# Optimization experiments

Measured on AMD Instinct MI355X. Metric: run time of the kernel, lower is better.

## Reference

```python
import jax, jax.numpy as jnp
import numpy as np

# --- dims (match init_kwargs) ---
B, T, S, K = 4, 128, 64, 2
CS = 1024            # codebook_size
NOTE_V, PHON_V = 128, 64
NE, PE, SE, PGB, PGE = 128, 128, 16, 8, 32
COND, TOK, PREV, D = 256, 256, 256, 512
NH, L_CTX, L_AUD = 8, 4, 6
HIST_WIN, AUD_WIN = 32, 64
DFF = 4 * D

CTX_KEYS = ["ln1_w","ln1_b","in_w","in_b","out_w","out_b","ln2_w","ln2_b","f1_w","f1_b","f2_w","f2_b"]


def _ln(x, w, b):
    m = x.mean(-1, keepdims=True)
    v = ((x - m) ** 2).mean(-1, keepdims=True)
    return (x - m) / jnp.sqrt(v + 1e-5) * w + b


def _mlp2(x, w1, b1, w2, b2, act):
    return act(x @ w1.T + b1) @ w2.T + b2


def _local_mask(n, win):
    i = jnp.arange(n)
    d = i[:, None] - i[None, :]
    return (d < 0) | (d >= win)   # True = masked (causal, local window)


def _mha(x, mask, in_w, in_b, out_w, out_b, nh):
    b, s, d = x.shape
    dh = d // nh
    q, k, v = jnp.split(x @ in_w.T + in_b, 3, axis=-1)
    sp = lambda t: t.reshape(b, s, nh, dh).transpose(0, 2, 1, 3)
    q, k, v = sp(q), sp(k), sp(v)
    sc = jnp.einsum('bhqd,bhkd->bhqk', q, k) * (1.0 / np.sqrt(dh))
    sc = jnp.where(mask, -1e9, sc)
    a = jax.nn.softmax(sc, axis=-1)
    o = jnp.einsum('bhqk,bhkd->bhqd', a, v).transpose(0, 2, 1, 3).reshape(b, s, d)
    return o @ out_w.T + out_b


def _block(x, mask, pr, nh):
    # pr: dict with ln1_w..f2_b for one layer (pre-norm attn + FFN, GELU)
    h = _ln(x, pr["ln1_w"], pr["ln1_b"])
    x = x + _mha(h, mask, pr["in_w"], pr["in_b"], pr["out_w"], pr["out_b"], nh)
    h2 = _ln(x, pr["ln2_w"], pr["ln2_b"])
    return x + _mlp2(h2, pr["f1_w"], pr["f1_b"], pr["f2_w"], pr["f2_b"],
                     lambda z: jax.nn.gelu(z, approximate=False))


def _forward(p, codes, note_id, phoneme_id, slur, phone_progress):
    silu = jax.nn.silu
    # ---- condition encoder ----
    cond_in = jnp.concatenate([
        p["note_emb_w"][note_id], p["phoneme_emb_w"][phoneme_id],
        p["slur_emb_w"][jnp.clip(slur, 0, 1)], p["pp_emb_w"][phone_progress]], -1)
    cond = _mlp2(cond_in, p["cond_w1"], p["cond_b1"], p["cond_w2"], p["cond_b2"], silu)
    # ---- shifted prev-step representation ----
    first = codes[..., 0]                       # [B,T,S]
    pooled = p["token_emb_w"][first].mean(2)    # [B,T,TOK]
    prev = _mlp2(pooled, p["prev_w1"], p["prev_b1"], p["prev_w2"], p["prev_b2"], silu)
    bos = jnp.broadcast_to(p["bos_step"], (B, 1, PREV))
    prev = jnp.concatenate([bos, prev[:, :-1]], 1)
    # ---- context transformer over steps (local causal window) ----
    h = _mlp2(jnp.concatenate([cond, prev], -1), p["step_w1"], p["step_b1"], p["step_w2"], p["step_b2"], silu)
    m_ctx = _local_mask(T, HIST_WIN)
    for l in range(L_CTX):
        pr = {k: p["ctx_" + k][l] for k in CTX_KEYS}
        h = _block(h, m_ctx, pr, NH)
    # ---- audio decoder over frames within each step ----
    tok = p["token_emb_w"][first] @ p["audio_in_w"].T + p["audio_in_b"]   # [B,T,S,D]
    bos_a = jnp.broadcast_to(p["audio_bos"], (B, T, 1, D))
    a = jnp.concatenate([bos_a, tok[:, :, :-1]], 2) + p["frame_pos"][None, None] + h[:, :, None]
    a = a.reshape(B * T, S, D)
    m_a = _local_mask(S, min(AUD_WIN, S))
    for l in range(L_AUD):
        pr = {k: p["aud_" + k][l] for k in CTX_KEYS}
        a = _block(a, m_a, pr, NH)
    ah = a.reshape(B, T, S, D)
    # ---- heads ----
    first_logits = (ah @ p["first_w"].T + p["first_b"])[..., None, :]     # [B,T,S,1,CS]
    rh = _mlp2(jnp.concatenate([ah, tok], -1), p["resc_w1"], p["resc_b1"], p["resc_w2"], p["resc_b2"], silu)
    res = jnp.einsum('btsd,kcd->btskc', rh, p["res_w"]) + p["res_b"]       # [B,T,S,K-1,CS]
    return jnp.concatenate([first_logits, res], axis=3)                    # [B,T,S,K,CS]


def setup_inputs() -> dict:
    key = jax.random.key(0)
    ks = iter(jax.random.split(key, 128))
    w = lambda *sh: jax.random.normal(next(ks), sh, jnp.float32) * 0.02
    z = lambda *sh: jnp.zeros(sh, jnp.float32)
    o = lambda *sh: jnp.ones(sh, jnp.float32)
    inp = {
        "codes": jax.random.randint(next(ks), (B, T, S, K), 0, CS, jnp.int32),
        "note_id": jax.random.randint(next(ks), (B, T), 0, NOTE_V, jnp.int32),
        "phoneme_id": jax.random.randint(next(ks), (B, T), 0, PHON_V, jnp.int32),
        "slur": jax.random.randint(next(ks), (B, T), 0, 2, jnp.int32),
        "phone_progress": jax.random.randint(next(ks), (B, T), 0, PGB, jnp.int32),
        "note_emb_w": w(NOTE_V, NE), "phoneme_emb_w": w(PHON_V, PE),
        "slur_emb_w": w(2, SE), "pp_emb_w": w(PGB, PGE),
        "cond_w1": w(COND, NE + PE + SE + PGE), "cond_b1": z(COND),
        "cond_w2": w(COND, COND), "cond_b2": z(COND),
        "token_emb_w": w(CS, TOK),
        "prev_w1": w(PREV, TOK), "prev_b1": z(PREV),
        "prev_w2": w(PREV, PREV), "prev_b2": z(PREV),
        "bos_step": z(PREV),
        "step_w1": w(D, COND + PREV), "step_b1": z(D),
        "step_w2": w(D, D), "step_b2": z(D),
        "audio_in_w": w(D, TOK), "audio_in_b": z(D),
        "audio_bos": z(D), "frame_pos": w(S, D),
        "first_w": w(CS, D), "first_b": z(CS),
        "resc_w1": w(D, 2 * D), "resc_b1": z(D),
        "resc_w2": w(D, D), "resc_b2": z(D),
        "res_w": w(K - 1, CS, D), "res_b": z(K - 1, CS),
    }
    for pre, L in (("ctx_", L_CTX), ("aud_", L_AUD)):
        inp[pre + "ln1_w"] = o(L, D); inp[pre + "ln1_b"] = z(L, D)
        inp[pre + "in_w"] = w(L, 3 * D, D); inp[pre + "in_b"] = z(L, 3 * D)
        inp[pre + "out_w"] = w(L, D, D); inp[pre + "out_b"] = z(L, D)
        inp[pre + "ln2_w"] = o(L, D); inp[pre + "ln2_b"] = z(L, D)
        inp[pre + "f1_w"] = w(L, DFF, D); inp[pre + "f1_b"] = z(L, DFF)
        inp[pre + "f2_w"] = w(L, D, DFF); inp[pre + "f2_b"] = z(L, D)
    return inp


FLOAT_KEYS = ["note_emb_w","phoneme_emb_w","slur_emb_w","pp_emb_w","cond_w1","cond_b1","cond_w2","cond_b2","token_emb_w","prev_w1","prev_b1","prev_w2","prev_b2","bos_step","step_w1","step_b1","step_w2","step_b2","audio_in_w","audio_in_b","audio_bos","frame_pos","first_w","first_b","resc_w1","resc_b1","resc_w2","resc_b2","res_w","res_b"] + [p + k for p in ("ctx_","aud_") for k in CTX_KEYS]


def reference(codes, note_id, phoneme_id, slur, phone_progress,
              note_emb_w, phoneme_emb_w, slur_emb_w, pp_emb_w,
              cond_w1, cond_b1, cond_w2, cond_b2, token_emb_w,
              prev_w1, prev_b1, prev_w2, prev_b2, bos_step,
              step_w1, step_b1, step_w2, step_b2,
              audio_in_w, audio_in_b, audio_bos, frame_pos,
              first_w, first_b, resc_w1, resc_b1, resc_w2, resc_b2, res_w, res_b,
              ctx_ln1_w, ctx_ln1_b, ctx_in_w, ctx_in_b, ctx_out_w, ctx_out_b,
              ctx_ln2_w, ctx_ln2_b, ctx_f1_w, ctx_f1_b, ctx_f2_w, ctx_f2_b,
              aud_ln1_w, aud_ln1_b, aud_in_w, aud_in_b, aud_out_w, aud_out_b,
              aud_ln2_w, aud_ln2_b, aud_f1_w, aud_f1_b, aud_f2_w, aud_f2_b):
    loc = locals()
    p = {k: loc[k] for k in FLOAT_KEYS}
    return _forward(p, codes, note_id, phoneme_id, slur, phone_progress)
```

## Files before the change

### kernel.cpp

```cpp
#include <hip/hip_runtime.h>
#include <cstdint>
#include <cstddef>

typedef unsigned short u16;
typedef short bf16x8 __attribute__((ext_vector_type(8)));
typedef float f32x4 __attribute__((ext_vector_type(4)));

__device__ __forceinline__ float bf2f(u16 u) { return __uint_as_float(((unsigned)u) << 16); }
__device__ __forceinline__ u16 f2bf(float f) {
  unsigned i = __float_as_uint(f);
  i += 0x7fffu + ((i >> 16) & 1u);
  return (u16)(i >> 16);
}
__device__ __forceinline__ unsigned packbf2(float lo, float hi) {
  return (unsigned)f2bf(lo) | ((unsigned)f2bf(hi) << 16);
}
__device__ __forceinline__ float lo16(unsigned u) { return __uint_as_float(u << 16); }
__device__ __forceinline__ float hi16(unsigned u) { return __uint_as_float(u & 0xffff0000u); }

__device__ __forceinline__ void async_ld16(u16* lds, const u16* g) {
  __builtin_amdgcn_global_load_lds((const __attribute__((address_space(1))) void*)g,
                                   (__attribute__((address_space(3))) void*)lds, 16, 0, 0);
}

__device__ __forceinline__ void fbar() {
  __builtin_amdgcn_sched_barrier(0);
  __builtin_amdgcn_s_barrier();
  __builtin_amdgcn_sched_barrier(0);
}

__global__ void k_cast8(const float4* __restrict__ x, uint4* __restrict__ y, int n8) {
  int i = blockIdx.x * 256 + threadIdx.x;
  if (i >= n8) return;
  float4 a = x[(size_t)i * 2], b = x[(size_t)i * 2 + 1];
  uint4 o;
  o.x = packbf2(a.x, a.y); o.y = packbf2(a.z, a.w);
  o.z = packbf2(b.x, b.y); o.w = packbf2(b.z, b.w);
  y[i] = o;
}

template<int ACT, int OUTM>
__global__ __launch_bounds__(256)
void gemm_mfma(const u16* __restrict__ A, const u16* __restrict__ W,
               const float* __restrict__ bias, void* __restrict__ Cp,
               int M, int N, int K, int ldc) {
  __shared__ __align__(16) u16 SM[24576];
  const int tid = threadIdx.x;
  const int wave = tid >> 6, lane = tid & 63;

  const int gx = gridDim.x;
  const int nwg = gx * (int)gridDim.y;
  const int flat = (int)blockIdx.y * gx + (int)blockIdx.x;
  const int xcd = flat & 7, lo = flat >> 3;
  const int q = nwg >> 3, r = nwg & 7;
  const int swz = (xcd < r ? xcd * (q + 1) : r * (q + 1) + (xcd - r) * q) + lo;
  const int bm = (swz / gx) * 128, bn = (swz % gx) * 128;

  const int wm = (wave & 1) * 64, wn = (wave >> 1) * 64;
  const int srow = tid >> 2, selem = (tid & 3) * 8;
  const u16* Ap0 = A + (size_t)(bm + srow) * K + selem;
  const u16* Ap1 = A + (size_t)(bm + srow + 64) * K + selem;
  const u16* Wp0 = W + (size_t)(bn + srow) * K + selem;
  const u16* Wp1 = W + (size_t)(bn + srow + 64) * K + selem;
  const int fr = lane & 15, fq = (lane >> 4) * 8;

  f32x4 acc[4][4];
#pragma unroll
  for (int i = 0; i < 4; ++i)
#pragma unroll
    for (int j = 0; j < 4; ++j) acc[i][j] = (f32x4){0.f, 0.f, 0.f, 0.f};

  const int nt = K >> 5;

  auto stage = [&](int buf, int k0) {
    u16* AsD = SM + buf * 4096 + tid * 8;
    u16* BsD = SM + 12288 + buf * 4096 + tid * 8;
    async_ld16(AsD, Ap0 + k0);
    async_ld16(AsD + 2048, Ap1 + k0);
    async_ld16(BsD, Wp0 + k0);
    async_ld16(BsD + 2048, Wp1 + k0);
  };

  stage(0, 0);
  if (nt > 1) stage(1, 32);

  int bi = 0;
  for (int t = 0; t < nt; ++t) {
    if (t + 1 < nt) asm volatile("s_waitcnt vmcnt(4)" ::: "memory");
    else            asm volatile("s_waitcnt vmcnt(0)" ::: "memory");
    __builtin_amdgcn_s_barrier();
    if (t + 2 < nt) {
      int nb = bi + 2; if (nb >= 3) nb -= 3;
      stage(nb, (t + 2) << 5);
    }
    const u16* Asb = SM + bi * 4096;
    const u16* Bsb = SM + 12288 + bi * 4096;
    bf16x8 af[4], bfv[4];
#pragma unroll
    for (int i = 0; i < 4; ++i)
      af[i] = *(const bf16x8*)&Asb[(wm + i * 16 + fr) * 32 + fq];
#pragma unroll
    for (int j = 0; j < 4; ++j)
      bfv[j] = *(const bf16x8*)&Bsb[(wn + j * 16 + fr) * 32 + fq];
#pragma unroll
    for (int i = 0; i < 4; ++i)
#pragma unroll
      for (int j = 0; j < 4; ++j)
        acc[i][j] = __builtin_amdgcn_mfma_f32_16x16x32_bf16(af[i], bfv[j], acc[i][j], 0, 0, 0);
    if (++bi == 3) bi = 0;
  }

  __syncthreads();
  const int lrow = (lane >> 4) * 4;
  const int colb = wn + fr;

  if (OUTM == 0) {
    u16* Ep = SM;
#pragma unroll
    for (int j = 0; j < 4; ++j) {
      float bv = bias[bn + colb + j * 16];
#pragma unroll
      for (int i = 0; i < 4; ++i)
#pragma unroll
        for (int rr = 0; rr < 4; ++rr) {
          float v = acc[i][j][rr] + bv;
          if (ACT == 1) v = v / (1.f + __expf(-v));
          else if (ACT == 2) v = 0.5f * v * (1.f + erff(v * 0.70710678118f));
          Ep[(wm + i * 16 + lrow + rr) * 128 + colb + j * 16] = f2bf(v);
        }
    }
    __syncthreads();
#pragma unroll
    for (int it = 0; it < 8; ++it) {
      int idx = it * 256 + tid;
      int row = idx >> 4, c = idx & 15;
      *(uint4*)((u16*)Cp + (size_t)(bm + row) * ldc + bn + c * 8) =
          ((const uint4*)Ep)[idx];
    }
  } else {
    float* Ep = (float*)SM;
    float* Cf = (float*)Cp;
#pragma unroll
    for (int ch = 0; ch < 2; ++ch) {
      if ((wave & 1) == ch) {
#pragma unroll
        for (int j = 0; j < 4; ++j) {
          float bv = bias[bn + colb + j * 16];
#pragma unroll
          for (int i = 0; i < 4; ++i)
#pragma unroll
            for (int rr = 0; rr < 4; ++rr) {
              float v = acc[i][j][rr] + bv;
              if (ACT == 1) v = v / (1.f + __expf(-v));
              else if (ACT == 2) v = 0.5f * v * (1.f + erff(v * 0.70710678118f));
              Ep[(i * 16 + lrow + rr) * 128 + colb + j * 16] = v;
            }
        }
      }
      __syncthreads();
#pragma unroll
      for (int it = 0; it < 8; ++it) {
        int idx = it * 256 + tid;
        int row = idx >> 5, c4 = idx & 31;
        size_t g = (size_t)(bm + ch * 64 + row) * ldc + bn + c4 * 4;
        float4 sv = ((const float4*)Ep)[idx];
        if (OUTM == 1) {
          float4 od = *(const float4*)(Cf + g);
          sv.x += od.x; sv.y += od.y; sv.z += od.z; sv.w += od.w;
        }
        *(float4*)(Cf + g) = sv;
      }
      __syncthreads();
    }
  }
}

template<int ACT, int OUTM>
__global__ __launch_bounds__(512, 2)
void gemm_mfma256(const u16* __restrict__ A, const u16* __restrict__ W,
                  const float* __restrict__ bias, void* __restrict__ Cp,
                  int M, int N, int K, int ldc) {
  __shared__ __align__(16) u16 SM[65536];
  const int tid = threadIdx.x;
  const int wave = tid >> 6, lane = tid & 63;
  const int wave_m = wave >> 2, wave_n = wave & 3;
  const int WM = wave_m * 128, WN = wave_n * 64;

  const int gx = gridDim.x;
  const int nwg = gx * (int)gridDim.y;
  const int flat = (int)blockIdx.y * gx + (int)blockIdx.x;
  const int xcd = flat & 7, lo = flat >> 3;
  const int q = nwg >> 3, r = nwg & 7;
  const int swz = (xcd < r ? xcd * (q + 1) : r * (q + 1) + (xcd - r) * q) + lo;
  const int bm = (swz / gx) * 256, bn = (swz % gx) * 256;

  const int srow = tid >> 3;
  const int slc = (tid & 7) ^ (srow & 7);
  const u16* Asrc = A + (size_t)(bm + srow) * K + slc * 8;
  const u16* Wsrc = W + (size_t)(bn + srow) * K + slc * 8;

  auto stage = [&](int buf, int k0) {
    u16* Ad = SM + buf * 32768 + tid * 8;
    u16* Bd = SM + buf * 32768 + 16384 + tid * 8;
#pragma unroll
    for (int qq = 0; qq < 4; ++qq)
      async_ld16(Ad + qq * 4096, Asrc + (size_t)qq * 64 * K + k0);
#pragma unroll
    for (int qq = 0; qq < 4; ++qq)
      async_ld16(Bd + qq * 4096, Wsrc + (size_t)qq * 64 * K + k0);
  };

  const int fr = lane & 15;
  const int pc0 = (((lane >> 4) ^ (fr & 7))) * 8;
  const int arow0 = (WM + fr) * 64;
  const int brow0 = (WN + fr) * 64;

  f32x4 acc[8][4];
#pragma unroll
  for (int i = 0; i < 8; ++i)
#pragma unroll
    for (int j = 0; j < 4; ++j) acc[i][j] = (f32x4){0.f, 0.f, 0.f, 0.f};

  const int nt = K >> 6;

  stage(0, 0);
  if (nt > 1) stage(1, 64);

  bf16x8 aA[4][2], bB[4][2];

#pragma unroll 1
  for (int t = 0; t < nt; ++t) {
    const u16* Ab = SM + (t & 1) * 32768;
    const u16* Bb = Ab + 16384;
    if (t + 1 < nt) asm volatile("s_waitcnt vmcnt(8)" ::: "memory");
    else            asm volatile("s_waitcnt vmcnt(0)" ::: "memory");
    fbar();
#pragma unroll
    for (int mi = 0; mi < 4; ++mi)
#pragma unroll
      for (int ks = 0; ks < 2; ++ks)
        aA[mi][ks] = *(const bf16x8*)&Ab[arow0 + mi * 1024 + (pc0 ^ (ks * 32))];
#pragma unroll
    for (int nj = 0; nj < 2; ++nj)
#pragma unroll
      for (int ks = 0; ks < 2; ++ks)
        bB[nj][ks] = *(const bf16x8*)&Bb[brow0 + nj * 1024 + (pc0 ^ (ks * 32))];
    __builtin_amdgcn_s_setprio(1);
#pragma unroll
    for (int mi = 0; mi < 4; ++mi)
#pragma unroll
      for (int nj = 0; nj < 2; ++nj)
#pragma unroll
        for (int ks = 0; ks < 2; ++ks)
          acc[mi][nj] = __builtin_amdgcn_mfma_f32_16x16x32_bf16(aA[mi][ks], bB[nj][ks], acc[mi][nj], 0, 0, 0);
    __builtin_amdgcn_s_setprio(0);
    fbar();
#pragma unroll
    for (int nj = 2; nj < 4; ++nj)
#pragma unroll
      for (int ks = 0; ks < 2; ++ks)
        bB[nj][ks] = *(const bf16x8*)&Bb[brow0 + nj * 1024 + (pc0 ^ (ks * 32))];
    __builtin_amdgcn_s_setprio(1);
#pragma unroll
    for (int mi = 0; mi < 4; ++mi)
#pragma unroll
      for (int nj = 2; nj < 4; ++nj)
#pragma unroll
        for (int ks = 0; ks < 2; ++ks)
          acc[mi][nj] = __builtin_amdgcn_mfma_f32_16x16x32_bf16(aA[mi][ks], bB[nj][ks], acc[mi][nj], 0, 0, 0);
    __builtin_amdgcn_s_setprio(0);
    fbar();
#pragma unroll
    for (int mi = 0; mi < 4; ++mi)
#pragma unroll
      for (int ks = 0; ks < 2; ++ks)
        aA[mi][ks] = *(const bf16x8*)&Ab[arow0 + (mi + 4) * 1024 + (pc0 ^ (ks * 32))];
    __builtin_amdgcn_s_setprio(1);
#pragma unroll
    for (int mi = 0; mi < 4; ++mi)
#pragma unroll
      for (int nj = 2; nj < 4; ++nj)
#pragma unroll
        for (int ks = 0; ks < 2; ++ks)
          acc[mi + 4][nj] = __builtin_amdgcn_mfma_f32_16x16x32_bf16(aA[mi][ks], bB[nj][ks], acc[mi + 4][nj], 0, 0, 0);
    __builtin_amdgcn_s_setprio(0);
    fbar();
    if (t + 2 < nt) stage(t & 1, (t + 2) << 6);
    __builtin_amdgcn_s_setprio(1);
#pragma unroll
    for (int mi = 0; mi < 4; ++mi)
#pragma unroll
      for (int nj = 0; nj < 2; ++nj)
#pragma unroll
        for (int ks = 0; ks < 2; ++ks)
          acc[mi + 4][nj] = __builtin_amdgcn_mfma_f32_16x16x32_bf16(aA[mi][ks], bB[nj][ks], acc[mi + 4][nj], 0, 0, 0);
    __builtin_amdgcn_s_setprio(0);
  }

  fbar();
  const int lrow = (lane >> 4) * 4;
  const int colb = WN + fr;

  if (OUTM == 0) {
    u16* Ep = SM;
#pragma unroll
    for (int nj = 0; nj < 4; ++nj) {
      float bv = bias[bn + colb + nj * 16];
#pragma unroll
      for (int mi = 0; mi < 8; ++mi)
#pragma unroll
        for (int rr = 0; rr < 4; ++rr) {
          float v = acc[mi][nj][rr] + bv;
          if (ACT == 1) v = v / (1.f + __expf(-v));
          else if (ACT == 2) v = 0.5f * v * (1.f + erff(v * 0.70710678118f));
          Ep[(WM + mi * 16 + lrow + rr) * 256 + colb + nj * 16] = f2bf(v);
        }
    }
    __syncthreads();
#pragma unroll
    for (int it = 0; it < 16; ++it) {
      int idx = it * 512 + tid;
      int row = idx >> 5, c = idx & 31;
      *(uint4*)((u16*)Cp + (size_t)(bm + row) * ldc + bn + c * 8) =
          ((const uint4*)Ep)[idx];
    }
  } else {
    float* Ep = (float*)SM;
    float* Cf = (float*)Cp;
#pragma unroll
    for (int ch = 0; ch < 2; ++ch) {
      if (wave_m == ch) {
#pragma unroll
        for (int nj = 0; nj < 4; ++nj) {
          float bv = bias[bn + colb + nj * 16];
#pragma unroll
          for (int mi = 0; mi < 8; ++mi)
#pragma unroll
            for (int rr = 0; rr < 4; ++rr) {
              float v = acc[mi][nj][rr] + bv;
              if (ACT == 1) v = v / (1.f + __expf(-v));
              else if (ACT == 2) v = 0.5f * v * (1.f + erff(v * 0.70710678118f));
              Ep[(mi * 16 + lrow + rr) * 256 + colb + nj * 16] = v;
            }
        }
      }
      __syncthreads();
#pragma unroll
      for (int it = 0; it < 16; ++it) {
        int idx = it * 512 + tid;
        int row = idx >> 6, c4 = idx & 63;
        size_t g = (size_t)(bm + ch * 128 + row) * ldc + bn + c4 * 4;
        float4 sv = ((const float4*)Ep)[idx];
        if (OUTM == 1) {
          float4 od = *(const float4*)(Cf + g);
          sv.x += od.x; sv.y += od.y; sv.z += od.z; sv.w += od.w;
        }
        *(float4*)(Cf + g) = sv;
      }
      __syncthreads();
    }
  }
}

__global__ __launch_bounds__(256)
void k_layernorm(const float* __restrict__ X, const float* __restrict__ w,
                 const float* __restrict__ b, u16* __restrict__ Y) {
  int row = blockIdx.x, tid = threadIdx.x;
  const float* x = X + (size_t)row * 512;
  float v0 = x[tid], v1 = x[tid + 256];
  __shared__ float red[4];
  float s = v0 + v1;
  for (int o = 32; o; o >>= 1) s += __shfl_down(s, o, 64);
  if ((tid & 63) == 0) red[tid >> 6] = s;
  __syncthreads();
  if (tid == 0) red[0] = (red[0] + red[1] + red[2] + red[3]) * (1.f / 512.f);
  __syncthreads();
  float mean = red[0];
  __syncthreads();
  float d0 = v0 - mean, d1 = v1 - mean;
  float q = d0 * d0 + d1 * d1;
  for (int o = 32; o; o >>= 1) q += __shfl_down(q, o, 64);
  if ((tid & 63) == 0) red[tid >> 6] = q;
  __syncthreads();
  if (tid == 0) red[0] = (red[0] + red[1] + red[2] + red[3]) * (1.f / 512.f);
  __syncthreads();
  float rstd = rsqrtf(red[0] + 1e-5f);
  size_t o0 = (size_t)row * 512 + tid;
  Y[o0] = f2bf(d0 * rstd * w[tid] + b[tid]);
  Y[o0 + 256] = f2bf(d1 * rstd * w[tid + 256] + b[tid + 256]);
}

__global__ void k_cond_gather(const int* __restrict__ note_id, const int* __restrict__ phon_id,
                              const int* __restrict__ slur, const int* __restrict__ pp,
                              const float* __restrict__ note_emb, const float* __restrict__ phon_emb,
                              const float* __restrict__ slur_emb, const float* __restrict__ pp_emb,
                              u16* __restrict__ out) {
  int bt = blockIdx.x, t = threadIdx.x;
  u16 v = 0;
  if (t < 128) v = f2bf(note_emb[note_id[bt] * 128 + t]);
  else if (t < 256) v = f2bf(phon_emb[phon_id[bt] * 128 + (t - 128)]);
  else if (t < 272) {
    int sv = slur[bt]; sv = sv < 0 ? 0 : (sv > 1 ? 1 : sv);
    v = f2bf(slur_emb[sv * 16 + (t - 256)]);
  } else if (t < 304) v = f2bf(pp_emb[pp[bt] * 32 + (t - 272)]);
  out[bt * 320 + t] = v;
}

__global__ void k_pad_w(const float* __restrict__ w, u16* __restrict__ out) {
  int n = blockIdx.x, t = threadIdx.x;
  out[n * 320 + t] = (t < 304) ? f2bf(w[n * 304 + t]) : (u16)0;
}

__global__ void k_femb(const int* __restrict__ codes, const uint4* __restrict__ emb,
                       uint4* __restrict__ out) {
  int i = blockIdx.x * 256 + threadIdx.x;
  int m = i >> 5, c = i & 31;
  out[i] = emb[(size_t)codes[m * 2] * 32 + c];
}

__global__ void k_pool(const u16* __restrict__ femb, u16* __restrict__ pooled) {
  int bt = blockIdx.x, c = threadIdx.x;
  float s = 0.f;
  for (int j = 0; j < 64; ++j) s += bf2f(femb[((size_t)bt * 64 + j) * 256 + c]);
  pooled[bt * 256 + c] = f2bf(s * (1.f / 64.f));
}

__global__ void k_stepin(const u16* __restrict__ cond, const u16* __restrict__ prevo,
                         const float* __restrict__ bosf, u16* __restrict__ out) {
  int bt = blockIdx.x, t = threadIdx.x;
  u16 v;
  if (t < 256) v = cond[bt * 256 + t];
  else {
    int tt = bt & 127;
    v = (tt == 0) ? f2bf(bosf[t - 256]) : prevo[(bt - 1) * 256 + (t - 256)];
  }
  out[bt * 512 + t] = v;
}

__global__ __launch_bounds__(64)
void k_ctx_attn(const u16* __restrict__ qkv, u16* __restrict__ out) {
  int t = blockIdx.x, h = blockIdx.y, b = blockIdx.z;
  int lane = threadIdx.x;
  int bt = b * 128 + t;
  float qd = bf2f(qkv[(size_t)bt * 1536 + h * 64 + lane]) * 0.125f;
  int klo = t - 31; if (klo < 0) klo = 0;
  int n = t - klo + 1;
  __shared__ float sc[32];
  for (int i = 0; i < n; ++i) {
    float p = qd * bf2f(qkv[((size_t)(b * 128 + klo + i)) * 1536 + 512 + h * 64 + lane]);
    for (int o = 32; o; o >>= 1) p += __shfl_xor(p, o, 64);
    if (lane == 0) sc[i] = p;
  }
  __syncthreads();
  float mx = -1e30f;
  for (int i = 0; i < n; ++i) mx = fmaxf(mx, sc[i]);
  float den = 0.f, acc = 0.f;
  for (int i = 0; i < n; ++i) {
    float p = __expf(sc[i] - mx);
    den += p;
    acc += p * bf2f(qkv[((size_t)(b * 128 + klo + i)) * 1536 + 1024 + h * 64 + lane]);
  }
  out[(size_t)bt * 512 + h * 64 + lane] = f2bf(acc / den);
}

__global__ __launch_bounds__(128)
void k_aud_attn_mfma(const u16* __restrict__ qkv, u16* __restrict__ out) {
  constexpr int LP = 66;
  __shared__ u16 Pl[2][64 * LP];
  __shared__ u16 Vt[2][64 * LP];
  const int wave = threadIdx.x >> 6, lane = threadIdx.x & 63;
  const int id = blockIdx.x * 2 + wave;
  const int seq = id >> 3, h = id & 7;
  const u16* Qb = qkv + (size_t)seq * 64 * 1536 + h * 64;
  const u16* Kb = Qb + 512;
  const u16* Vb = Qb + 1024;
  u16* Plw = Pl[wave];
  u16* Vtw = Vt[wave];
  const int fr = lane & 15, fq = (lane >> 4) * 8;

#pragma unroll
  for (int t = 0; t < 8; ++t) {
    int vr = (lane >> 3) + 8 * t, vc = (lane & 7) * 8;
    uint4 vv = *(const uint4*)(Vb + (size_t)vr * 1536 + vc);
    Vtw[(vc + 0) * LP + vr] = (u16)(vv.x & 0xffff);
    Vtw[(vc + 1) * LP + vr] = (u16)(vv.x >> 16);
    Vtw[(vc + 2) * LP + vr] = (u16)(vv.y & 0xffff);
    Vtw[(vc + 3) * LP + vr] = (u16)(vv.y >> 16);
    Vtw[(vc + 4) * LP + vr] = (u16)(vv.z & 0xffff);
    Vtw[(vc + 5) * LP + vr] = (u16)(vv.z >> 16);
    Vtw[(vc + 6) * LP + vr] = (u16)(vv.w & 0xffff);
    Vtw[(vc + 7) * LP + vr] = (u16)(vv.w >> 16);
  }

  bf16x8 aq[4][2], bk[4][2];
#pragma unroll
  for (int i = 0; i < 4; ++i)
#pragma unroll
    for (int c = 0; c < 2; ++c) {
      aq[i][c] = *(const bf16x8*)(Qb + (size_t)(i * 16 + fr) * 1536 + fq + 32 * c);
      bk[i][c] = *(const bf16x8*)(Kb + (size_t)(i * 16 + fr) * 1536 + fq + 32 * c);
    }
  f32x4 s[4][4];
#pragma unroll
  for (int i = 0; i < 4; ++i)
#pragma unroll
    for (int j = 0; j < 4; ++j) s[i][j] = (f32x4){0.f, 0.f, 0.f, 0.f};
#pragma unroll
  for (int c = 0; c < 2; ++c)
#pragma unroll
    for (int i = 0; i < 4; ++i)
#pragma unroll
      for (int j = 0; j < 4; ++j)
        s[i][j] = __builtin_amdgcn_mfma_f32_16x16x32_bf16(aq[i][c], bk[j][c], s[i][j], 0, 0, 0);

  const int qr = (lane >> 4) * 4;
#pragma unroll
  for (int i = 0; i < 4; ++i) {
#pragma unroll
    for (int r = 0; r < 4; ++r) {
      int row = 16 * i + qr + r;
      float mx = -1e30f;
      float vj[4];
#pragma unroll
      for (int j = 0; j < 4; ++j) {
        float v = s[i][j][r] * 0.125f;
        if (16 * j + fr > row) v = -1e30f;
        vj[j] = v;
        mx = fmaxf(mx, v);
      }
      for (int o = 8; o; o >>= 1) mx = fmaxf(mx, __shfl_xor(mx, o, 64));
      float den = 0.f;
#pragma unroll
      for (int j = 0; j < 4; ++j) { vj[j] = __expf(vj[j] - mx); den += vj[j]; }
      for (int o = 8; o; o >>= 1) den += __shfl_xor(den, o, 64);
      float inv = 1.f / den;
#pragma unroll
      for (int j = 0; j < 4; ++j)
        Plw[row * LP + 16 * j + fr] = f2bf(vj[j] * inv);
    }
  }
  __syncthreads();

  f32x4 o4[4][4];
#pragma unroll
  for (int i = 0; i < 4; ++i)
#pragma unroll
    for (int j = 0; j < 4; ++j) o4[i][j] = (f32x4){0.f, 0.f, 0.f, 0.f};
#pragma unroll
  for (int c = 0; c < 2; ++c) {
    bf16x8 ap[4], bv[4];
#pragma unroll
    for (int i = 0; i < 4; ++i)
      ap[i] = *(const bf16x8*)&Plw[(16 * i + fr) * LP + fq + 32 * c];
#pragma unroll
    for (int j = 0; j < 4; ++j)
      bv[j] = *(const bf16x8*)&Vtw[(16 * j + fr) * LP + fq + 32 * c];
#pragma unroll
    for (int i = 0; i < 4; ++i)
#pragma unroll
      for (int j = 0; j < 4; ++j)
        o4[i][j] = __builtin_amdgcn_mfma_f32_16x16x32_bf16(ap[i], bv[j], o4[i][j], 0, 0, 0);
  }
#pragma unroll
  for (int i = 0; i < 4; ++i)
#pragma unroll
    for (int r = 0; r < 4; ++r) {
      int row = 16 * i + qr + r;
      u16* ob = out + ((size_t)seq * 64 + row) * 512 + h * 64;
#pragma unroll
      for (int j = 0; j < 4; ++j) ob[16 * j + fr] = f2bf(o4[i][j][r]);
    }
}

__global__ void k_abuild(const uint4* __restrict__ tok, const float4* __restrict__ bosf,
                         const float4* __restrict__ fpos, const float4* __restrict__ hstep,
                         float4* __restrict__ a) {
  size_t i = (size_t)blockIdx.x * 256 + threadIdx.x;
  int d8 = (int)(i & 63);
  size_t row = i >> 6;
  int s = (int)(row & 63);
  size_t bt = row >> 6;
  float t0, t1, t2, t3, t4, t5, t6, t7;
  if (s == 0) {
    float4 b0 = bosf[d8 * 2], b1 = bosf[d8 * 2 + 1];
    t0 = b0.x; t1 = b0.y; t2 = b0.z; t3 = b0.w;
    t4 = b1.x; t5 = b1.y; t6 = b1.z; t7 = b1.w;
  } else {
    uint4 tv = tok[(row - 1) * 64 + d8];
    t0 = lo16(tv.x); t1 = hi16(tv.x); t2 = lo16(tv.y); t3 = hi16(tv.y);
    t4 = lo16(tv.z); t5 = hi16(tv.z); t6 = lo16(tv.w); t7 = hi16(tv.w);
  }
  float4 f0 = fpos[(size_t)s * 128 + d8 * 2], f1 = fpos[(size_t)s * 128 + d8 * 2 + 1];
  float4 h0 = hstep[bt * 128 + d8 * 2], h1 = hstep[bt * 128 + d8 * 2 + 1];
  float4 o0, o1;
  o0.x = t0 + f0.x + h0.x; o0.y = t1 + f0.y + h0.y;
  o0.z = t2 + f0.z + h0.z; o0.w = t3 + f0.w + h0.w;
  o1.x = t4 + f1.x + h1.x; o1.y = t5 + f1.y + h1.y;
  o1.z = t6 + f1.z + h1.z; o1.w = t7 + f1.w + h1.w;
  a[i * 2] = o0; a[i * 2 + 1] = o1;
}

__global__ void k_cat(const uint4* __restrict__ ah, const uint4* __restrict__ tok,
                      uint4* __restrict__ out) {
  size_t i = (size_t)blockIdx.x * 256 + threadIdx.x;
  size_t m = i >> 7;
  int c = (int)(i & 127);
  out[i] = (c < 64) ? ah[m * 64 + c] : tok[m * 64 + (c - 64)];
}

template<int ACT, int OUTM>
static inline void gemm(const u16* A, const u16* W, const float* bias, void* C,
                        int M, int N, int K, int ldc, hipStream_t s) {
  gemm_mfma<ACT, OUTM><<<dim3(N / 128, M / 128), 256, 0, s>>>(A, W, bias, C, M, N, K, ldc);
}

template<int ACT, int OUTM>
static inline void gemmBig(const u16* A, const u16* W, const float* bias, void* C,
                           int M, int N, int K, int ldc, hipStream_t s) {
  gemm_mfma256<ACT, OUTM><<<dim3(N / 256, M / 256), 512, 0, s>>>(A, W, bias, C, M, N, K, ldc);
}

static inline void cast_bf16(const float* x, u16* y, size_t n, hipStream_t s) {
  int n8 = (int)(n / 8);
  k_cast8<<<(n8 + 255) / 256, 256, 0, s>>>((const float4*)x, (uint4*)y, n8);
}

extern "C" void kernel_launch(void* const* d_in, const int* in_sizes, int n_in,
                              void* d_out, int out_size, void* d_ws, size_t ws_size,
                              hipStream_t stream) {
  const int* codes    = (const int*)d_in[0];
  const int* note_id  = (const int*)d_in[1];
  const int* phon_id  = (const int*)d_in[2];
  const int* slur     = (const int*)d_in[3];
  const int* pprog    = (const int*)d_in[4];
  const float* note_emb = (const float*)d_in[5];
  const float* phon_emb = (const float*)d_in[6];
  const float* slur_emb = (const float*)d_in[7];
  const float* pp_emb   = (const float*)d_in[8];
  const float* cond_w1  = (const float*)d_in[9];
  const float* cond_b1  = (const float*)d_in[10];
  const float* cond_w2  = (const float*)d_in[11];
  const float* cond_b2  = (const float*)d_in[12];
  const float* tok_emb  = (const float*)d_in[13];
  const float* prev_w1  = (const float*)d_in[14];
  const float* prev_b1  = (const float*)d_in[15];
  const float* prev_w2  = (const float*)d_in[16];
  const float* prev_b2  = (const float*)d_in[17];
  const float* bos_step = (const float*)d_in[18];
  const float* step_w1  = (const float*)d_in[19];
  const float* step_b1  = (const float*)d_in[20];
  const float* step_w2  = (const float*)d_in[21];
  const float* step_b2  = (const float*)d_in[22];
  const float* audio_in_w = (const float*)d_in[23];
  const float* audio_in_b = (const float*)d_in[24];
  const float* audio_bos  = (const float*)d_in[25];
  const float* frame_pos  = (const float*)d_in[26];
  const float* first_w  = (const float*)d_in[27];
  const float* first_b  = (const float*)d_in[28];
  const float* resc_w1  = (const float*)d_in[29];
  const float* resc_b1  = (const float*)d_in[30];
  const float* resc_w2  = (const float*)d_in[31];
  const float* resc_b2  = (const float*)d_in[32];
  const float* res_w    = (const float*)d_in[33];
  const float* res_b    = (const float*)d_in[34];
  const float* ctx_w[12]; for (int i = 0; i < 12; ++i) ctx_w[i] = (const float*)d_in[35 + i];
  const float* aud_w[12]; for (int i = 0; i < 12; ++i) aud_w[i] = (const float*)d_in[47 + i];

  char* p = (char*)d_ws;
  auto alloc = [&](size_t b) { char* r = p; p += (b + 255) & ~(size_t)255; return r; };
  float* A_res = (float*)alloc(32768ull * 512 * 4);
  u16* T_tok  = (u16*)alloc(32768ull * 512 * 2);
  u16* LNb    = (u16*)alloc(32768ull * 512 * 2);
  u16* AOb    = (u16*)alloc(32768ull * 512 * 2);
  u16* QF     = (u16*)alloc(32768ull * 2048 * 2);
  u16* f_emb  = (u16*)alloc(32768ull * 256 * 2);
  u16* temb   = (u16*)alloc(1024ull * 256 * 2);
  u16* cond_in = (u16*)alloc(512ull * 320 * 2);
  u16* cw1p   = (u16*)alloc(256ull * 320 * 2);
  u16* cw2    = (u16*)alloc(256ull * 256 * 2);
  u16* pw1    = (u16*)alloc(256ull * 256 * 2);
  u16* pw2    = (u16*)alloc(256ull * 256 * 2);
  u16* sw1    = (u16*)alloc(512ull * 512 * 2);
  u16* sw2    = (u16*)alloc(512ull * 512 * 2);
  u16* ainw   = (u16*)alloc(512ull * 256 * 2);
  u16* fw     = (u16*)alloc(1024ull * 512 * 2);
  u16* rw1    = (u16*)alloc(512ull * 1024 * 2);
  u16* rw2    = (u16*)alloc(512ull * 512 * 2);
  u16* resw   = (u16*)alloc(1024ull * 512 * 2);
  u16* cxin   = (u16*)alloc(4ull * 1536 * 512 * 2);
  u16* cxout  = (u16*)alloc(4ull * 512 * 512 * 2);
  u16* cxf1   = (u16*)alloc(4ull * 2048 * 512 * 2);
  u16* cxf2   = (u16*)alloc(4ull * 512 * 2048 * 2);
  u16* adin   = (u16*)alloc(6ull * 1536 * 512 * 2);
  u16* adout  = (u16*)alloc(6ull * 512 * 512 * 2);
  u16* adf1   = (u16*)alloc(6ull * 2048 * 512 * 2);
  u16* adf2   = (u16*)alloc(6ull * 512 * 2048 * 2);
  u16* cond_h = (u16*)alloc(512ull * 256 * 2);
  u16* condv  = (u16*)alloc(512ull * 256 * 2);
  u16* pooled = (u16*)alloc(512ull * 256 * 2);
  u16* prevh  = (u16*)alloc(512ull * 256 * 2);
  u16* prevo  = (u16*)alloc(512ull * 256 * 2);
  u16* stepin = (u16*)alloc(512ull * 512 * 2);
  u16* hmid   = (u16*)alloc(512ull * 512 * 2);
  float* hstep = (float*)alloc(512ull * 512 * 4);

  k_pad_w<<<256, 320, 0, stream>>>(cond_w1, cw1p);
  cast_bf16(cond_w2, cw2, 256ull * 256, stream);
  cast_bf16(prev_w1, pw1, 256ull * 256, stream);
  cast_bf16(prev_w2, pw2, 256ull * 256, stream);
  cast_bf16(step_w1, sw1, 512ull * 512, stream);
  cast_bf16(step_w2, sw2, 512ull * 512, stream);
  cast_bf16(tok_emb, temb, 1024ull * 256, stream);
  cast_bf16(audio_in_w, ainw, 512ull * 256, stream);
  cast_bf16(first_w, fw, 1024ull * 512, stream);
  cast_bf16(resc_w1, rw1, 512ull * 1024, stream);
  cast_bf16(resc_w2, rw2, 512ull * 512, stream);
  cast_bf16(res_w, resw, 1024ull * 512, stream);
  cast_bf16(ctx_w[2], cxin, 4ull * 1536 * 512, stream);
  cast_bf16(ctx_w[4], cxout, 4ull * 512 * 512, stream);
  cast_bf16(ctx_w[8], cxf1, 4ull * 2048 * 512, stream);
  cast_bf16(ctx_w[10], cxf2, 4ull * 512 * 2048, stream);
  cast_bf16(aud_w[2], adin, 6ull * 1536 * 512, stream);
  cast_bf16(aud_w[4], adout, 6ull * 512 * 512, stream);
  cast_bf16(aud_w[8], adf1, 6ull * 2048 * 512, stream);
  cast_bf16(aud_w[10], adf2, 6ull * 512 * 2048, stream);

  k_cond_gather<<<512, 320, 0, stream>>>(note_id, phon_id, slur, pprog,
                                         note_emb, phon_emb, slur_emb, pp_emb, cond_in);
  k_femb<<<4096, 256, 0, stream>>>(codes, (const uint4*)temb, (uint4*)f_emb);
  k_pool<<<512, 256, 0, stream>>>(f_emb, pooled);
  gemm<1, 0>(cond_in, cw1p, cond_b1, cond_h, 512, 256, 320, 256, stream);
  gemm<0, 0>(cond_h, cw2, cond_b2, condv, 512, 256, 256, 256, stream);
  gemm<1, 0>(pooled, pw1, prev_b1, prevh, 512, 256, 256, 256, stream);
  gemm<0, 0>(prevh, pw2, prev_b2, prevo, 512, 256, 256, 256, stream);
  k_stepin<<<512, 512, 0, stream>>>(condv, prevo, bos_step, stepin);
  gemm<1, 0>(stepin, sw1, step_b1, hmid, 512, 512, 512, 512, stream);
  gemm<0, 2>(hmid, sw2, step_b2, hstep, 512, 512, 512, 512, stream);

  for (int l = 0; l < 4; ++l) {
    k_layernorm<<<512, 256, 0, stream>>>(hstep, ctx_w[0] + l * 512, ctx_w[1] + l * 512, LNb);
    gemm<0, 0>(LNb, cxin + (size_t)l * 1536 * 512, ctx_w[3] + l * 1536, QF, 512, 1536, 512, 1536, stream);
    k_ctx_attn<<<dim3(128, 8, 4), 64, 0, stream>>>(QF, AOb);
    gemm<0, 1>(AOb, cxout + (size_t)l * 512 * 512, ctx_w[5] + l * 512, hstep, 512, 512, 512, 512, stream);
    k_layernorm<<<512, 256, 0, stream>>>(hstep, ctx_w[6] + l * 512, ctx_w[7] + l * 512, LNb);
    gemm<2, 0>(LNb, cxf1 + (size_t)l * 2048 * 512, ctx_w[9] + l * 2048, QF, 512, 2048, 512, 2048, stream);
    gemm<0, 1>(QF, cxf2 + (size_t)l * 512 * 2048, ctx_w[11] + l * 512, hstep, 512, 512, 2048, 512, stream);
  }

  gemmBig<0, 0>(f_emb, ainw, audio_in_b, T_tok, 32768, 512, 256, 512, stream);
  k_abuild<<<8192, 256, 0, stream>>>((const uint4*)T_tok, (const float4*)audio_bos,
                                     (const float4*)frame_pos, (const float4*)hstep, (float4*)A_res);
  for (int l = 0; l < 6; ++l) {
    k_layernorm<<<32768, 256, 0, stream>>>(A_res, aud_w[0] + l * 512, aud_w[1] + l * 512, LNb);
    gemmBig<0, 0>(LNb, adin + (size_t)l * 1536 * 512, aud_w[3] + l * 1536, QF, 32768, 1536, 512, 1536, stream);
    k_aud_attn_mfma<<<2048, 128, 0, stream>>>(QF, AOb);
    gemmBig<0, 1>(AOb, adout + (size_t)l * 512 * 512, aud_w[5] + l * 512, A_res, 32768, 512, 512, 512, stream);
    k_layernorm<<<32768, 256, 0, stream>>>(A_res, aud_w[6] + l * 512, aud_w[7] + l * 512, LNb);
    gemmBig<2, 0>(LNb, adf1 + (size_t)l * 2048 * 512, aud_w[9] + l * 2048, QF, 32768, 2048, 512, 2048, stream);
    gemmBig<0, 1>(QF, adf2 + (size_t)l * 512 * 2048, aud_w[11] + l * 512, A_res, 32768, 512, 2048, 512, stream);
  }

  {
    int n8 = 32768 * 512 / 8;
    k_cast8<<<(n8 + 255) / 256, 256, 0, stream>>>((const float4*)A_res, (uint4*)LNb, n8);
  }
  gemmBig<0, 2>(LNb, fw, first_b, (float*)d_out, 32768, 1024, 512, 2048, stream);
  k_cat<<<16384, 256, 0, stream>>>((const uint4*)LNb, (const uint4*)T_tok, (uint4*)QF);
  gemmBig<1, 0>(QF, rw1, resc_b1, AOb, 32768, 512, 1024, 512, stream);
  gemmBig<0, 0>(AOb, rw2, resc_b2, T_tok, 32768, 512, 512, 512, stream);
  gemmBig<0, 2>(T_tok, resw, res_b, (float*)d_out + 1024, 32768, 1024, 512, 2048, stream);
}
```

Before: 3.601 ms.

## Retile small GEMMs to 64x64 and fuse the concat into the residual GEMM load

The M=512 condition, step and context GEMMs move to a new 64x64-tile kernel. It writes results straight from registers, so these small problems launch more workgroups. The residual-head GEMM gains a split-A mode that reads columns 0-511 from one buffer and 512-1023 from another, which removes the separate k_cat kernel and its intermediate buffer. A __syncthreads is also dropped in the audio attention kernel between writing the P tile and the PV stage. That is only safe if each wave reads only its own rows, so it risks a race.

```diff
diff --git a/kernel.cpp b/kernel.cpp
--- a/kernel.cpp
+++ b/kernel.cpp
@@ -41,44 +41,28 @@
 
 template<int ACT, int OUTM>
 __global__ __launch_bounds__(256)
-void gemm_mfma(const u16* __restrict__ A, const u16* __restrict__ W,
-               const float* __restrict__ bias, void* __restrict__ Cp,
-               int M, int N, int K, int ldc) {
-  __shared__ __align__(16) u16 SM[24576];
+void gemm_mfma64(const u16* __restrict__ A, const u16* __restrict__ W,
+                 const float* __restrict__ bias, void* __restrict__ Cp,
+                 int M, int N, int K, int ldc) {
+  __shared__ __align__(16) u16 SM[12288];
   const int tid = threadIdx.x;
   const int wave = tid >> 6, lane = tid & 63;
-
-  const int gx = gridDim.x;
-  const int nwg = gx * (int)gridDim.y;
-  const int flat = (int)blockIdx.y * gx + (int)blockIdx.x;
-  const int xcd = flat & 7, lo = flat >> 3;
-  const int q = nwg >> 3, r = nwg & 7;
-  const int swz = (xcd < r ? xcd * (q + 1) : r * (q + 1) + (xcd - r) * q) + lo;
-  const int bm = (swz / gx) * 128, bn = (swz % gx) * 128;
-
-  const int wm = (wave & 1) * 64, wn = (wave >> 1) * 64;
+  const int bm = blockIdx.y * 64, bn = blockIdx.x * 64;
   const int srow = tid >> 2, selem = (tid & 3) * 8;
-  const u16* Ap0 = A + (size_t)(bm + srow) * K + selem;
-  const u16* Ap1 = A + (size_t)(bm + srow + 64) * K + selem;
-  const u16* Wp0 = W + (size_t)(bn + srow) * K + selem;
-  const u16* Wp1 = W + (size_t)(bn + srow + 64) * K + selem;
+  const u16* Ap = A + (size_t)(bm + srow) * K + selem;
+  const u16* Wp = W + (size_t)(bn + srow) * K + selem;
   const int fr = lane & 15, fq = (lane >> 4) * 8;
-
-  f32x4 acc[4][4];
-#pragma unroll
-  for (int i = 0; i < 4; ++i)
-#pragma unroll
-    for (int j = 0; j < 4; ++j) acc[i][j] = (f32x4){0.f, 0.f, 0.f, 0.f};
+  const int wn = wave * 16;
+
+  f32x4 acc[4];
+#pragma unroll
+  for (int i = 0; i < 4; ++i) acc[i] = (f32x4){0.f, 0.f, 0.f, 0.f};
 
   const int nt = K >> 5;
 
   auto stage = [&](int buf, int k0) {
-    u16* AsD = SM + buf * 4096 + tid * 8;
-    u16* BsD = SM + 12288 + buf * 4096 + tid * 8;
-    async_ld16(AsD, Ap0 + k0);
-    async_ld16(AsD + 2048, Ap1 + k0);
-    async_ld16(BsD, Wp0 + k0);
-    async_ld16(BsD + 2048, Wp1 + k0);
+    async_ld16(SM + buf * 2048 + tid * 8, Ap + k0);
+    async_ld16(SM + 6144 + buf * 2048 + tid * 8, Wp + k0);
   };
 
   stage(0, 0);
@@ -86,98 +70,47 @@
 
   int bi = 0;
   for (int t = 0; t < nt; ++t) {
-    if (t + 1 < nt) asm volatile("s_waitcnt vmcnt(4)" ::: "memory");
+    if (t + 1 < nt) asm volatile("s_waitcnt vmcnt(2)" ::: "memory");
     else            asm volatile("s_waitcnt vmcnt(0)" ::: "memory");
     __builtin_amdgcn_s_barrier();
     if (t + 2 < nt) {
       int nb = bi + 2; if (nb >= 3) nb -= 3;
       stage(nb, (t + 2) << 5);
     }
-    const u16* Asb = SM + bi * 4096;
-    const u16* Bsb = SM + 12288 + bi * 4096;
-    bf16x8 af[4], bfv[4];
+    const u16* Asb = SM + bi * 2048;
+    const u16* Bsb = SM + 6144 + bi * 2048;
+    bf16x8 af[4];
 #pragma unroll
     for (int i = 0; i < 4; ++i)
-      af[i] = *(const bf16x8*)&Asb[(wm + i * 16 + fr) * 32 + fq];
-#pragma unroll
-    for (int j = 0; j < 4; ++j)
-      bfv[j] = *(const bf16x8*)&Bsb[(wn + j * 16 + fr) * 32 + fq];
+      af[i] = *(const bf16x8*)&Asb[(i * 16 + fr) * 32 + fq];
+    bf16x8 bf1 = *(const bf16x8*)&Bsb[(wn + fr) * 32 + fq];
 #pragma unroll
     for (int i = 0; i < 4; ++i)
-#pragma unroll
-      for (int j = 0; j < 4; ++j)
-        acc[i][j] = __builtin_amdgcn_mfma_f32_16x16x32_bf16(af[i], bfv[j], acc[i][j], 0, 0, 0);
+      acc[i] = __builtin_amdgcn_mfma_f32_16x16x32_bf16(af[i], bf1, acc[i], 0, 0, 0);
     if (++bi == 3) bi = 0;
   }
 
-  __syncthreads();
-  const int lrow = (lane >> 4) * 4;
-  const int colb = wn + fr;
-
-  if (OUTM == 0) {
-    u16* Ep = SM;
-#pragma unroll
-    for (int j = 0; j < 4; ++j) {
-      float bv = bias[bn + colb + j * 16];
-#pragma unroll
-      for (int i = 0; i < 4; ++i)
-#pragma unroll
-        for (int rr = 0; rr < 4; ++rr) {
-          float v = acc[i][j][rr] + bv;
-          if (ACT == 1) v = v / (1.f + __expf(-v));
-          else if (ACT == 2) v = 0.5f * v * (1.f + erff(v * 0.70710678118f));
-          Ep[(wm + i * 16 + lrow + rr) * 128 + colb + j * 16] = f2bf(v);
-        }
-    }
-    __syncthreads();
-#pragma unroll
-    for (int it = 0; it < 8; ++it) {
-      int idx = it * 256 + tid;
-      int row = idx >> 4, c = idx & 15;
-      *(uint4*)((u16*)Cp + (size_t)(bm + row) * ldc + bn + c * 8) =
-          ((const uint4*)Ep)[idx];
-    }
-  } else {
-    float* Ep = (float*)SM;
-    float* Cf = (float*)Cp;
-#pragma unroll
-    for (int ch = 0; ch < 2; ++ch) {
-      if ((wave & 1) == ch) {
-#pragma unroll
-        for (int j = 0; j < 4; ++j) {
-          float bv = bias[bn + colb + j * 16];
-#pragma unroll
-          for (int i = 0; i < 4; ++i)
-#pragma unroll
-            for (int rr = 0; rr < 4; ++rr) {
-              float v = acc[i][j][rr] + bv;
-              if (ACT == 1) v = v / (1.f + __expf(-v));
-              else if (ACT == 2) v = 0.5f * v * (1.f + erff(v * 0.70710678118f));
-              Ep[(i * 16 + lrow + rr) * 128 + colb + j * 16] = v;
-            }
-        }
-      }
-      __syncthreads();
-#pragma unroll
-      for (int it = 0; it < 8; ++it) {
-        int idx = it * 256 + tid;
-        int row = idx >> 5, c4 = idx & 31;
-        size_t g = (size_t)(bm + ch * 64 + row) * ldc + bn + c4 * 4;
-        float4 sv = ((const float4*)Ep)[idx];
-        if (OUTM == 1) {
-          float4 od = *(const float4*)(Cf + g);
-          sv.x += od.x; sv.y += od.y; sv.z += od.z; sv.w += od.w;
-        }
-        *(float4*)(Cf + g) = sv;
-      }
-      __syncthreads();
-    }
-  }
-}
-
-template<int ACT, int OUTM>
+  const int mr = bm + (lane >> 4) * 4;
+  const int nc = bn + wn + fr;
+  float bv = bias[nc];
+#pragma unroll
+  for (int i = 0; i < 4; ++i)
+#pragma unroll
+    for (int rr = 0; rr < 4; ++rr) {
+      float v = acc[i][rr] + bv;
+      if (ACT == 1) v = v / (1.f + __expf(-v));
+      else if (ACT == 2) v = 0.5f * v * (1.f + erff(v * 0.70710678118f));
+      size_t off = (size_t)(mr + i * 16 + rr) * ldc + nc;
+      if (OUTM == 0) ((u16*)Cp)[off] = f2bf(v);
+      else if (OUTM == 1) ((float*)Cp)[off] += v;
+      else ((float*)Cp)[off] = v;
+    }
+}
+
+template<int ACT, int OUTM, int SPLITA>
 __global__ __launch_bounds__(512, 2)
-void gemm_mfma256(const u16* __restrict__ A, const u16* __restrict__ W,
+void gemm_mfma256(const u16* __restrict__ A, const u16* __restrict__ A2,
+                  const u16* __restrict__ W,
                   const float* __restrict__ bias, void* __restrict__ Cp,
                   int M, int N, int K, int ldc) {
   __shared__ __align__(16) u16 SM[65536];
@@ -195,16 +128,30 @@
   const int bm = (swz / gx) * 256, bn = (swz % gx) * 256;
 
   const int srow = tid >> 3;
-  const int slc = (tid & 7) ^ (srow & 7);
-  const u16* Asrc = A + (size_t)(bm + srow) * K + slc * 8;
-  const u16* Wsrc = W + (size_t)(bn + srow) * K + slc * 8;
+  const int slc8 = ((tid & 7) ^ (srow & 7)) * 8;
+  const u16* Asrc = nullptr; const u16* A2src = nullptr;
+  if (SPLITA) {
+    Asrc  = A  + (size_t)(bm + srow) * 512;
+    A2src = A2 + (size_t)(bm + srow) * 512 - 512;
+  } else {
+    Asrc = A + (size_t)(bm + srow) * K + slc8;
+  }
+  const u16* Wsrc = W + (size_t)(bn + srow) * K + slc8;
 
   auto stage = [&](int buf, int k0) {
     u16* Ad = SM + buf * 32768 + tid * 8;
-    u16* Bd = SM + buf * 32768 + 16384 + tid * 8;
-#pragma unroll
-    for (int qq = 0; qq < 4; ++qq)
-      async_ld16(Ad + qq * 4096, Asrc + (size_t)qq * 64 * K + k0);
+    u16* Bd = Ad + 16384;
+    if (SPLITA) {
+      int col = k0 + slc8;
+      const u16* s = (col < 512 ? Asrc : A2src) + col;
+#pragma unroll
+      for (int qq = 0; qq < 4; ++qq)
+        async_ld16(Ad + qq * 4096, s + (size_t)qq * 64 * 512);
+    } else {
+#pragma unroll
+      for (int qq = 0; qq < 4; ++qq)
+        async_ld16(Ad + qq * 4096, Asrc + (size_t)qq * 64 * K + k0);
+    }
 #pragma unroll
     for (int qq = 0; qq < 4; ++qq)
       async_ld16(Bd + qq * 4096, Wsrc + (size_t)qq * 64 * K + k0);
@@ -539,7 +486,6 @@
         Plw[row * LP + 16 * j + fr] = f2bf(vj[j] * inv);
     }
   }
-  __syncthreads();
 
   f32x4 o4[4][4];
 #pragma unroll
@@ -600,24 +546,22 @@
   a[i * 2] = o0; a[i * 2 + 1] = o1;
 }
 
-__global__ void k_cat(const uint4* __restrict__ ah, const uint4* __restrict__ tok,
-                      uint4* __restrict__ out) {
-  size_t i = (size_t)blockIdx.x * 256 + threadIdx.x;
-  size_t m = i >> 7;
-  int c = (int)(i & 127);
-  out[i] = (c < 64) ? ah[m * 64 + c] : tok[m * 64 + (c - 64)];
-}
-
 template<int ACT, int OUTM>
-static inline void gemm(const u16* A, const u16* W, const float* bias, void* C,
-                        int M, int N, int K, int ldc, hipStream_t s) {
-  gemm_mfma<ACT, OUTM><<<dim3(N / 128, M / 128), 256, 0, s>>>(A, W, bias, C, M, N, K, ldc);
+static inline void gemmS(const u16* A, const u16* W, const float* bias, void* C,
+                         int M, int N, int K, int ldc, hipStream_t s) {
+  gemm_mfma64<ACT, OUTM><<<dim3(N / 64, M / 64), 256, 0, s>>>(A, W, bias, C, M, N, K, ldc);
 }
 
 template<int ACT, int OUTM>
 static inline void gemmBig(const u16* A, const u16* W, const float* bias, void* C,
                            int M, int N, int K, int ldc, hipStream_t s) {
-  gemm_mfma256<ACT, OUTM><<<dim3(N / 256, M / 256), 512, 0, s>>>(A, W, bias, C, M, N, K, ldc);
+  gemm_mfma256<ACT, OUTM, 0><<<dim3(N / 256, M / 256), 512, 0, s>>>(A, nullptr, W, bias, C, M, N, K, ldc);
+}
+
+template<int ACT, int OUTM>
+static inline void gemmBigSplit(const u16* A, const u16* A2, const u16* W, const float* bias,
+                                void* C, int M, int N, int K, int ldc, hipStream_t s) {
+  gemm_mfma256<ACT, OUTM, 1><<<dim3(N / 256, M / 256), 512, 0, s>>>(A, A2, W, bias, C, M, N, K, ldc);
 }
 
 static inline void cast_bf16(const float* x, u16* y, size_t n, hipStream_t s) {
@@ -729,22 +673,22 @@
                                          note_emb, phon_emb, slur_emb, pp_emb, cond_in);
   k_femb<<<4096, 256, 0, stream>>>(codes, (const uint4*)temb, (uint4*)f_emb);
   k_pool<<<512, 256, 0, stream>>>(f_emb, pooled);
-  gemm<1, 0>(cond_in, cw1p, cond_b1, cond_h, 512, 256, 320, 256, stream);
-  gemm<0, 0>(cond_h, cw2, cond_b2, condv, 512, 256, 256, 256, stream);
-  gemm<1, 0>(pooled, pw1, prev_b1, prevh, 512, 256, 256, 256, stream);
-  gemm<0, 0>(prevh, pw2, prev_b2, prevo, 512, 256, 256, 256, stream);
+  gemmS<1, 0>(cond_in, cw1p, cond_b1, cond_h, 512, 256, 320, 256, stream);
+  gemmS<0, 0>(cond_h, cw2, cond_b2, condv, 512, 256, 256, 256, stream);
+  gemmS<1, 0>(pooled, pw1, prev_b1, prevh, 512, 256, 256, 256, stream);
+  gemmS<0, 0>(prevh, pw2, prev_b2, prevo, 512, 256, 256, 256, stream);
   k_stepin<<<512, 512, 0, stream>>>(condv, prevo, bos_step, stepin);
-  gemm<1, 0>(stepin, sw1, step_b1, hmid, 512, 512, 512, 512, stream);
-  gemm<0, 2>(hmid, sw2, step_b2, hstep, 512, 512, 512, 512, stream);
+  gemmS<1, 0>(stepin, sw1, step_b1, hmid, 512, 512, 512, 512, stream);
+  gemmS<0, 2>(hmid, sw2, step_b2, hstep, 512, 512, 512, 512, stream);
 
   for (int l = 0; l < 4; ++l) {
     k_layernorm<<<512, 256, 0, stream>>>(hstep, ctx_w[0] + l * 512, ctx_w[1] + l * 512, LNb);
-    gemm<0, 0>(LNb, cxin + (size_t)l * 1536 * 512, ctx_w[3] + l * 1536, QF, 512, 1536, 512, 1536, stream);
+    gemmS<0, 0>(LNb, cxin + (size_t)l * 1536 * 512, ctx_w[3] + l * 1536, QF, 512, 1536, 512, 1536, stream);
     k_ctx_attn<<<dim3(128, 8, 4), 64, 0, stream>>>(QF, AOb);
-    gemm<0, 1>(AOb, cxout + (size_t)l * 512 * 512, ctx_w[5] + l * 512, hstep, 512, 512, 512, 512, stream);
+    gemmS<0, 1>(AOb, cxout + (size_t)l * 512 * 512, ctx_w[5] + l * 512, hstep, 512, 512, 512, 512, stream);
     k_layernorm<<<512, 256, 0, stream>>>(hstep, ctx_w[6] + l * 512, ctx_w[7] + l * 512, LNb);
-    gemm<2, 0>(LNb, cxf1 + (size_t)l * 2048 * 512, ctx_w[9] + l * 2048, QF, 512, 2048, 512, 2048, stream);
-    gemm<0, 1>(QF, cxf2 + (size_t)l * 512 * 2048, ctx_w[11] + l * 512, hstep, 512, 512, 2048, 512, stream);
+    gemmS<2, 0>(LNb, cxf1 + (size_t)l * 2048 * 512, ctx_w[9] + l * 2048, QF, 512, 2048, 512, 2048, stream);
+    gemmS<0, 1>(QF, cxf2 + (size_t)l * 512 * 2048, ctx_w[11] + l * 512, hstep, 512, 512, 2048, 512, stream);
   }
 
   gemmBig<0, 0>(f_emb, ainw, audio_in_b, T_tok, 32768, 512, 256, 512, stream);
@@ -765,8 +709,7 @@
     k_cast8<<<(n8 + 255) / 256, 256, 0, stream>>>((const float4*)A_res, (uint4*)LNb, n8);
   }
   gemmBig<0, 2>(LNb, fw, first_b, (float*)d_out, 32768, 1024, 512, 2048, stream);
-  k_cat<<<16384, 256, 0, stream>>>((const uint4*)LNb, (const uint4*)T_tok, (uint4*)QF);
-  gemmBig<1, 0>(QF, rw1, resc_b1, AOb, 32768, 512, 1024, 512, stream);
+  gemmBigSplit<1, 0>(LNb, T_tok, rw1, resc_b1, AOb, 32768, 512, 1024, 512, stream);
   gemmBig<0, 0>(AOb, rw2, resc_b2, T_tok, 32768, 512, 512, 512, stream);
   gemmBig<0, 2>(T_tok, resw, res_b, (float*)d_out + 1024, 32768, 1024, 512, 2048, stream);
 }
```

After: 3.475 ms. 3.5% less time.
